# Kernel optimization log

Measured on AMD Instinct MI355X. Metric: run time of the kernel, lower is better.

Reference implementation:

```python
import jax, jax.numpy as jnp
import numpy as np

NP, NA = 200000, 100000        # paper / author node counts
EW, EC = 300000, 300000        # writes / cites edge counts
HID, H, D = 128, 4, 32         # hidden, heads, head dim
FIN_P, FIN_A, OUT = 256, 128, 16
SCALE = float(1.0 / np.sqrt(D))


def _seg_softmax(alpha, idx, n):
    # softmax over edges grouped by destination node (PyG softmax)
    m = jax.ops.segment_max(alpha, idx, num_segments=n)
    e = jnp.exp(alpha - m[idx])
    s = jax.ops.segment_sum(e, idx, num_segments=n)
    return e / (s[idx] + 1e-16)


def _edge_type(k_src, v_src, q_dst, src, dst, a_rel, m_rel, p_rel, n_dst):
    # per-relation transform at node level, then gather-attend-scatter
    kr = jnp.einsum('nhd,hde->nhe', k_src, a_rel)
    vr = jnp.einsum('nhd,hde->nhe', v_src, m_rel)
    alpha = jnp.sum(q_dst[dst] * kr[src], axis=-1) * p_rel * SCALE  # [E,H]
    alpha = _seg_softmax(alpha, dst, n_dst)
    return jax.ops.segment_sum(vr[src] * alpha[..., None], dst, num_segments=n_dst)


def setup_inputs() -> dict:
    key = jax.random.key(0)
    ks = iter(jax.random.split(key, 48))

    def nrm(shape, s=0.05):
        return jax.random.normal(next(ks), shape, jnp.float32) * s

    inp = dict(
        x_paper=nrm((NP, FIN_P), 1.0),
        x_author=nrm((NA, FIN_A), 1.0),
        writes_src=jax.random.randint(next(ks), (EW,), 0, NA, dtype=jnp.int32),
        writes_dst=jax.random.randint(next(ks), (EW,), 0, NP, dtype=jnp.int32),
        cites_src=jax.random.randint(next(ks), (EC,), 0, NP, dtype=jnp.int32),
        cites_dst=jax.random.randint(next(ks), (EC,), 0, NP, dtype=jnp.int32),
        lin_paper_w=nrm((FIN_P, HID)), lin_paper_b=jnp.zeros((HID,), jnp.float32),
        lin_author_w=nrm((FIN_A, HID)), lin_author_b=jnp.zeros((HID,), jnp.float32),
        lin_out_w=nrm((HID, OUT)), lin_out_b=jnp.zeros((OUT,), jnp.float32),
    )
    for t in ('paper', 'author'):
        for nm in ('k', 'q', 'v', 'a'):
            inp[f'{nm}_w_{t}'] = nrm((HID, HID))
            inp[f'{nm}_b_{t}'] = jnp.zeros((HID,), jnp.float32)
        inp[f'skip_{t}'] = jnp.ones((), jnp.float32)
    for e in ('writes', 'cites'):
        inp[f'a_rel_{e}'] = nrm((H, D, D), 0.18)
        inp[f'm_rel_{e}'] = nrm((H, D, D), 0.18)
        inp[f'p_rel_{e}'] = jnp.ones((H,), jnp.float32)
    return inp


def reference(x_paper, x_author, writes_src, writes_dst, cites_src, cites_dst,
              lin_paper_w, lin_paper_b, lin_author_w, lin_author_b,
              lin_out_w, lin_out_b,
              k_w_paper, k_b_paper, q_w_paper, q_b_paper, v_w_paper, v_b_paper,
              a_w_paper, a_b_paper, skip_paper,
              k_w_author, k_b_author, q_w_author, q_b_author, v_w_author, v_b_author,
              a_w_author, a_b_author, skip_author,
              a_rel_writes, m_rel_writes, p_rel_writes,
              a_rel_cites, m_rel_cites, p_rel_cites):
    # per-node-type input projection + relu
    hp = jax.nn.relu(x_paper @ lin_paper_w + lin_paper_b)
    ha = jax.nn.relu(x_author @ lin_author_w + lin_author_b)
    # HGTConv: per-node-type k/q/v, [N,H,D]
    k_p = (hp @ k_w_paper + k_b_paper).reshape(NP, H, D)
    q_p = (hp @ q_w_paper + q_b_paper).reshape(NP, H, D)
    v_p = (hp @ v_w_paper + v_b_paper).reshape(NP, H, D)
    k_a = (ha @ k_w_author + k_b_author).reshape(NA, H, D)
    v_a = (ha @ v_w_author + v_b_author).reshape(NA, H, D)
    # heterogeneous multi-relation attention, group='sum' over edge types
    out_p = _edge_type(k_a, v_a, q_p, writes_src, writes_dst,
                       a_rel_writes, m_rel_writes, p_rel_writes, NP)
    out_p = out_p + _edge_type(k_p, v_p, q_p, cites_src, cites_dst,
                               a_rel_cites, m_rel_cites, p_rel_cites, NP)
    # output projection + gated skip (paper type; only 'paper' feeds the head)
    op = jax.nn.gelu(out_p.reshape(NP, HID), approximate=False) @ a_w_paper + a_b_paper
    beta = jax.nn.sigmoid(skip_paper)
    hp = beta * op + (1.0 - beta) * hp
    return hp @ lin_out_w + lin_out_b  # [NP, OUT]
```

## Files before the change

kernel.cpp:

```cpp
#include <hip/hip_runtime.h>
#include <cstdint>

#define NP 200000
#define NA 100000
#define EW 300000
#define EC 300000
#define HID 128
#define FIN_P 256
#define FIN_A 128
#define NOUT 16
#define ATT_SCALE 0.17677669529663687f

#define NBP 1563
#define NBA 782

#define SCAN_N (2 * NP)
#define SCAN_BS 256
#define SCAN_ITEMS 4
#define SCAN_TILE 1024
#define SCAN_NB ((SCAN_N + SCAN_TILE - 1) / SCAN_TILE)

typedef short s8v __attribute__((ext_vector_type(8)));
typedef float f32x4 __attribute__((ext_vector_type(4)));
typedef unsigned short ushort_t;

__device__ __forceinline__ float gelu_f(float x) {
  return 0.5f * x * (1.0f + erff(x * 0.70710678118654752f));
}
__device__ __forceinline__ ushort_t f2bf(float f) {
  unsigned u = __float_as_uint(f);
  return (ushort_t)((u + 0x7FFFu + ((u >> 16) & 1u)) >> 16);
}
__device__ __forceinline__ unsigned pack2bf(float a, float b) {
  return (unsigned)f2bf(a) | ((unsigned)f2bf(b) << 16);
}
__device__ __forceinline__ unsigned cvtpk(float a, float b) {
  unsigned r;
  asm("v_cvt_pk_bf16_f32 %0, %1, %2" : "=v"(r) : "v"(a), "v"(b));
  return r;
}
__device__ __forceinline__ float bflo(unsigned u) { return __uint_as_float(u << 16); }
__device__ __forceinline__ float bfhi(unsigned u) { return __uint_as_float(u & 0xFFFF0000u); }

__device__ __forceinline__ void gl16(const void* g, void* l) {
  __builtin_amdgcn_global_load_lds(
      (const __attribute__((address_space(1))) void*)g,
      (__attribute__((address_space(3))) void*)l, 16, 0, 0);
}

__device__ __forceinline__ int s2row(int r) { return (r ^ (r >> 2)) & 3; }

__global__ void prep_all(
    const float* __restrict__ qw,  const float* __restrict__ qb,
    const float* __restrict__ kwp, const float* __restrict__ kbp, const float* __restrict__ arc,
    const float* __restrict__ vwp, const float* __restrict__ vbp, const float* __restrict__ mrc,
    const float* __restrict__ kwa, const float* __restrict__ kba, const float* __restrict__ arw,
    const float* __restrict__ vwa, const float* __restrict__ vba, const float* __restrict__ mrw,
    const float* __restrict__ lpw, const float* __restrict__ law,
    const float* __restrict__ aw, const float* __restrict__ ab,
    const float* __restrict__ skip, const float* __restrict__ W2, const float* __restrict__ b2,
    ushort_t* __restrict__ Wall, float* __restrict__ Ball,
    ushort_t* __restrict__ Wcatb, float* __restrict__ bo,
    int* __restrict__ cnt)
{
  const int b = blockIdx.x, tid = threadIdx.x;
  if (b == 0) {
    for (int idx = tid; idx < 16384; idx += 256) {
      int c = idx >> 7, r = idx & 127;
      Wall[idx] = f2bf(qw[r * 128 + c]);
    }
    for (int c = tid; c < 128; c += 256) Ball[c] = qb[c];
  } else if (b <= 4) {
    const float *W, *bias, *rel;
    switch (b) {
      case 1:  W = kwp; bias = kbp; rel = arc; break;
      case 2:  W = vwp; bias = vbp; rel = mrc; break;
      case 3:  W = kwa; bias = kba; rel = arw; break;
      default: W = vwa; bias = vba; rel = mrw; break;
    }
    for (int idx = tid; idx < 16384; idx += 256) {
      int c = idx >> 7, r = idx & 127, h = c >> 5, e = c & 31;
      float s = 0.f;
      #pragma unroll
      for (int d = 0; d < 32; ++d) s += W[r * 128 + h * 32 + d] * rel[h * 1024 + d * 32 + e];
      Wall[b * 16384 + idx] = f2bf(s);
    }
    for (int c = tid; c < 128; c += 256) {
      int h = c >> 5, e = c & 31;
      float s = 0.f;
      #pragma unroll
      for (int d = 0; d < 32; ++d) s += bias[h * 32 + d] * rel[h * 1024 + d * 32 + e];
      Ball[b * 128 + c] = s;
    }
  } else if (b == 5) {
    for (int idx = tid; idx < 16384; idx += 256) {
      int c = idx >> 7, r = idx & 127;
      Wall[5 * 16384 + idx] = f2bf(law[r * 128 + c]);
    }
  } else if (b == 6) {
    for (int idx = tid; idx < 32768; idx += 256) {
      int c = idx >> 8, r = idx & 255;
      Wall[6 * 16384 + idx] = f2bf(lpw[r * 128 + c]);
    }
  } else if (b == 7) {
    float beta = 1.0f / (1.0f + expf(-skip[0]));
    for (int idx = tid; idx < 4096; idx += 256) {
      int c = idx >> 8, k = idx & 255;
      float v;
      if (k < 128) {
        float s = 0.f;
        for (int j = 0; j < 128; ++j) s += aw[k * 128 + j] * W2[j * 16 + c];
        v = beta * s;
      } else {
        v = (1.0f - beta) * W2[(k - 128) * 16 + c];
      }
      Wcatb[c * 256 + k] = f2bf(v);
    }
    if (tid < 16) {
      float s = 0.f;
      for (int k = 0; k < 128; ++k) s += ab[k] * W2[k * 16 + tid];
      bo[tid] = beta * s + b2[tid];
    }
  } else {
    int chunk = SCAN_N / 8;
    int base = (b - 8) * chunk;
    for (int i = tid; i < chunk; i += 256) cnt[base + i] = 0;
  }
}

__global__ __launch_bounds__(256) void gemm_main(
    const float* __restrict__ xp, const float* __restrict__ xa,
    const ushort_t* __restrict__ Wall,
    const float* __restrict__ bp, const float* __restrict__ ba,
    const float* __restrict__ Ball,
    ushort_t* __restrict__ hpo, ushort_t* __restrict__ hao,
    ushort_t* __restrict__ qkv, ushort_t* __restrict__ kvw)
{
  __shared__ ushort_t As[16384];
  __shared__ ushort_t Bs[16384];
  const bool isP = blockIdx.x < NBP;
  const int bid = isP ? blockIdx.x : blockIdx.x - NBP;
  const float* A = isP ? xp : xa;
  const ushort_t* Wp = Wall + (isP ? 6 * 16384 : 5 * 16384);
  const float* biasp = isP ? bp : ba;
  ushort_t* Chp = isP ? hpo : hao;
  const int M = isP ? NP : NA;
  const int KT = isP ? 256 : 128;
  const int nt = KT >> 6;
  const int base_set = isP ? 0 : 3;
  const int nsets = isP ? 3 : 2;

  const int tid  = threadIdx.x;
  const int lane = tid & 63;
  const int wv   = tid >> 6;
  const int wr   = wv >> 1, wc = wv & 1;
  const int l15  = lane & 15, kgl = lane >> 4;
  const int s2l  = (l15 ^ (l15 >> 2)) & 3;
  const int row0 = bid * 128;

  const int r0 = tid >> 2, kgp = tid & 3;
  const int sk = kgp ^ s2row(r0);
  int g0 = row0 + r0;       if (g0 > M - 1) g0 = M - 1;
  int g1 = row0 + r0 + 64;  if (g1 > M - 1) g1 = M - 1;

  {
    const float* a0p = A + (size_t)g0 * KT + sk * 8;
    const float* a1p = A + (size_t)g1 * KT + sk * 8;
    const ushort_t* b0p = Wp + (size_t)r0 * KT + sk * 8;
    const ushort_t* b1p = Wp + (size_t)(r0 + 64) * KT + sk * 8;

    f32x4 acc[4][4];
    #pragma unroll
    for (int i = 0; i < 4; ++i)
      #pragma unroll
      for (int j = 0; j < 4; ++j) acc[i][j] = (f32x4){0.f, 0.f, 0.f, 0.f};

    for (int t = 0; t < nt; ++t) {
      const int kt = t * 64;
      gl16(b0p + kt,      &Bs[(size_t)tid * 8]);
      gl16(b1p + kt,      &Bs[(size_t)(tid + 256) * 8]);
      gl16(b0p + kt + 32, &Bs[(size_t)(tid + 512) * 8]);
      gl16(b1p + kt + 32, &Bs[(size_t)(tid + 768) * 8]);
      float4 fa0 = *(const float4*)(a0p + kt);
      float4 fa1 = *(const float4*)(a0p + kt + 4);
      float4 fa2 = *(const float4*)(a1p + kt);
      float4 fa3 = *(const float4*)(a1p + kt + 4);
      float4 fb0 = *(const float4*)(a0p + kt + 32);
      float4 fb1 = *(const float4*)(a0p + kt + 36);
      float4 fb2 = *(const float4*)(a1p + kt + 32);
      float4 fb3 = *(const float4*)(a1p + kt + 36);
      uint4 v;
      v.x = cvtpk(fa0.x, fa0.y); v.y = cvtpk(fa0.z, fa0.w);
      v.z = cvtpk(fa1.x, fa1.y); v.w = cvtpk(fa1.z, fa1.w);
      *(uint4*)&As[(size_t)tid * 8] = v;
      v.x = cvtpk(fa2.x, fa2.y); v.y = cvtpk(fa2.z, fa2.w);
      v.z = cvtpk(fa3.x, fa3.y); v.w = cvtpk(fa3.z, fa3.w);
      *(uint4*)&As[(size_t)(tid + 256) * 8] = v;
      v.x = cvtpk(fb0.x, fb0.y); v.y = cvtpk(fb0.z, fb0.w);
      v.z = cvtpk(fb1.x, fb1.y); v.w = cvtpk(fb1.z, fb1.w);
      *(uint4*)&As[(size_t)(tid + 512) * 8] = v;
      v.x = cvtpk(fb2.x, fb2.y); v.y = cvtpk(fb2.z, fb2.w);
      v.z = cvtpk(fb3.x, fb3.y); v.w = cvtpk(fb3.z, fb3.w);
      *(uint4*)&As[(size_t)(tid + 768) * 8] = v;
      __syncthreads();

      const s8v* As8 = (const s8v*)As;
      const s8v* Bs8 = (const s8v*)Bs;
      #pragma unroll
      for (int pg = 0; pg < 2; ++pg) {
        s8v af[4], bfv[4];
        #pragma unroll
        for (int i = 0; i < 4; ++i)
          af[i]  = As8[pg * 512 + (wr * 64 + i * 16 + l15) * 4 + (kgl ^ s2l)];
        #pragma unroll
        for (int j = 0; j < 4; ++j)
          bfv[j] = Bs8[pg * 512 + (wc * 64 + j * 16 + l15) * 4 + (kgl ^ s2l)];
        #pragma unroll
        for (int i = 0; i < 4; ++i)
          #pragma unroll
          for (int j = 0; j < 4; ++j)
            acc[i][j] = __builtin_amdgcn_mfma_f32_16x16x32_bf16(af[i], bfv[j], acc[i][j], 0, 0, 0);
      }
      __syncthreads();
    }

    float bv[4];
    #pragma unroll
    for (int j = 0; j < 4; ++j) bv[j] = biasp[wc * 64 + j * 16 + l15];
    #pragma unroll
    for (int i = 0; i < 4; ++i) {
      #pragma unroll
      for (int r = 0; r < 4; ++r) {
        int row = row0 + wr * 64 + i * 16 + kgl * 4 + r;
        if (row < M) {
          #pragma unroll
          for (int j = 0; j < 4; ++j) {
            float vv = acc[i][j][r] + bv[j];
            vv = fmaxf(vv, 0.f);
            Chp[(size_t)row * 128 + wc * 64 + j * 16 + l15] = f2bf(vv);
          }
        }
      }
    }
  }
  __syncthreads();

  {
    const ushort_t* a0h = Chp + (size_t)g0 * 128 + sk * 8;
    const ushort_t* a1h = Chp + (size_t)g1 * 128 + sk * 8;
    #pragma unroll
    for (int t = 0; t < 4; ++t) {
      gl16(a0h + t * 32, &As[((size_t)t * 512 + tid) * 8]);
      gl16(a1h + t * 32, &As[((size_t)t * 512 + tid + 256) * 8]);
    }

    for (int si = 0; si < nsets; ++si) {
      const int set = base_set + si;
      const ushort_t* W = Wall + set * 16384;
      const float* bias = Ball + set * 128;
      ushort_t* C = isP ? (qkv + (size_t)set * NP * HID)
                        : (kvw + (size_t)(set - 3) * NA * HID);
      const ushort_t* b0p = W + (size_t)r0 * 128 + sk * 8;
      const ushort_t* b1p = W + (size_t)(r0 + 64) * 128 + sk * 8;
      #pragma unroll
      for (int t = 0; t < 4; ++t) {
        gl16(b0p + t * 32, &Bs[((size_t)t * 512 + tid) * 8]);
        gl16(b1p + t * 32, &Bs[((size_t)t * 512 + tid + 256) * 8]);
      }
      __syncthreads();

      f32x4 acc[4][4];
      #pragma unroll
      for (int i = 0; i < 4; ++i)
        #pragma unroll
        for (int j = 0; j < 4; ++j) acc[i][j] = (f32x4){0.f, 0.f, 0.f, 0.f};

      const s8v* As8 = (const s8v*)As;
      const s8v* Bs8 = (const s8v*)Bs;
      #pragma unroll
      for (int t = 0; t < 4; ++t) {
        s8v af[4], bfv[4];
        #pragma unroll
        for (int i = 0; i < 4; ++i)
          af[i]  = As8[t * 512 + (wr * 64 + i * 16 + l15) * 4 + (kgl ^ s2l)];
        #pragma unroll
        for (int j = 0; j < 4; ++j)
          bfv[j] = Bs8[t * 512 + (wc * 64 + j * 16 + l15) * 4 + (kgl ^ s2l)];
        #pragma unroll
        for (int i = 0; i < 4; ++i)
          #pragma unroll
          for (int j = 0; j < 4; ++j)
            acc[i][j] = __builtin_amdgcn_mfma_f32_16x16x32_bf16(af[i], bfv[j], acc[i][j], 0, 0, 0);
      }

      float bv[4];
      #pragma unroll
      for (int j = 0; j < 4; ++j) bv[j] = bias[wc * 64 + j * 16 + l15];
      #pragma unroll
      for (int i = 0; i < 4; ++i) {
        #pragma unroll
        for (int r = 0; r < 4; ++r) {
          int row = row0 + wr * 64 + i * 16 + kgl * 4 + r;
          if (row < M) {
            #pragma unroll
            for (int j = 0; j < 4; ++j) {
              C[(size_t)row * 128 + wc * 64 + j * 16 + l15] = f2bf(acc[i][j][r] + bv[j]);
            }
          }
        }
      }
      __syncthreads();
    }
  }
}

__global__ void hist_k(const int* __restrict__ wdst, const int* __restrict__ cdst,
                       int* __restrict__ cnt)
{
  int t = blockIdx.x * blockDim.x + threadIdx.x;
  if (t < EW) atomicAdd(&cnt[wdst[t]], 1);
  if (t < EC) atomicAdd(&cnt[NP + cdst[t]], 1);
}

__global__ __launch_bounds__(SCAN_BS) void scan1(const int* __restrict__ cnt,
                                                 int* __restrict__ off,
                                                 int* __restrict__ bsum)
{
  __shared__ int sh[2][SCAN_BS];
  int tid = threadIdx.x;
  int base = blockIdx.x * SCAN_TILE + tid * SCAN_ITEMS;
  int v[SCAN_ITEMS]; int tsum = 0;
  #pragma unroll
  for (int i = 0; i < SCAN_ITEMS; ++i) {
    int idx = base + i;
    v[i] = (idx < SCAN_N) ? cnt[idx] : 0;
    tsum += v[i];
  }
  int p = 0;
  sh[0][tid] = tsum; __syncthreads();
  #pragma unroll
  for (int d = 1; d < SCAN_BS; d <<= 1) {
    int x = sh[p][tid] + ((tid >= d) ? sh[p][tid - d] : 0);
    sh[p ^ 1][tid] = x; __syncthreads(); p ^= 1;
  }
  int run = sh[p][tid] - tsum;
  #pragma unroll
  for (int i = 0; i < SCAN_ITEMS; ++i) {
    int idx = base + i;
    if (idx < SCAN_N) off[idx] = run;
    run += v[i];
  }
  if (tid == SCAN_BS - 1) bsum[blockIdx.x] = sh[p][tid];
}

__global__ __launch_bounds__(512) void scan2(int* __restrict__ bsum)
{
  __shared__ int sh[2][512];
  int tid = threadIdx.x;
  int v = (tid < SCAN_NB) ? bsum[tid] : 0;
  int p = 0;
  sh[0][tid] = v; __syncthreads();
  for (int d = 1; d < 512; d <<= 1) {
    int x = sh[p][tid] + ((tid >= d) ? sh[p][tid - d] : 0);
    sh[p ^ 1][tid] = x; __syncthreads(); p ^= 1;
  }
  if (tid < SCAN_NB) bsum[tid] = sh[p][tid] - v;
}

__global__ __launch_bounds__(SCAN_BS) void scan3(int* __restrict__ off, int* __restrict__ cur,
                                                 const int* __restrict__ bsum)
{
  int add = bsum[blockIdx.x];
  int base = blockIdx.x * SCAN_TILE + threadIdx.x;
  #pragma unroll
  for (int i = 0; i < SCAN_ITEMS; ++i) {
    int idx = base + i * SCAN_BS;
    if (idx < SCAN_N) { int t = off[idx] + add; off[idx] = t; cur[idx] = t; }
  }
  if (blockIdx.x == 0 && threadIdx.x == 0) off[SCAN_N] = EW + EC;
}

__global__ void fill_k(const int* __restrict__ wsrc, const int* __restrict__ wdst,
                       const int* __restrict__ csrc, const int* __restrict__ cdst,
                       int* __restrict__ cur, int* __restrict__ esrc)
{
  int t = blockIdx.x * blockDim.x + threadIdx.x;
  if (t < EW) { int p = atomicAdd(&cur[wdst[t]], 1); esrc[p] = wsrc[t] << 8; }
  if (t < EC) { int p = atomicAdd(&cur[NP + cdst[t]], 1); esrc[p] = csrc[t] << 8; }
}

__global__ __launch_bounds__(256) void node_attn(
    const int* __restrict__ off, const int* __restrict__ esrc,
    const ushort_t* __restrict__ q,
    const ushort_t* __restrict__ kr_w, const ushort_t* __restrict__ vr_w,
    const ushort_t* __restrict__ kr_c, const ushort_t* __restrict__ vr_c,
    const float* __restrict__ p_rel_w, const float* __restrict__ p_rel_c,
    ushort_t* __restrict__ out_p)
{
  int gid = blockIdx.x * blockDim.x + threadIdx.x;
  int node = gid >> 4;
  int l16 = gid & 15;
  int h = l16 >> 2;
  unsigned loff = (unsigned)(l16 * 16);

  int eb0 = off[node],      ee0 = off[node + 1];
  int eb1 = off[NP + node], ee1 = off[NP + node + 1];

  uint4 qv = *(const uint4*)(q + (size_t)node * HID + l16 * 8);

  int pi0 = (eb0 < ee0) ? eb0 : 0;
  int pi1 = (eb1 < ee1) ? eb1 : 0;
  unsigned pb0 = (unsigned)esrc[pi0] + loff;
  unsigned pb1 = (unsigned)esrc[pi1] + loff;
  uint4 pk[2], pv[2];
  pk[0] = *(const uint4*)((const char*)kr_w + pb0);
  pv[0] = *(const uint4*)((const char*)vr_w + pb0);
  pk[1] = *(const uint4*)((const char*)kr_c + pb1);
  pv[1] = *(const uint4*)((const char*)vr_c + pb1);

  float qf[8];
  {
    const unsigned* pq = (const unsigned*)&qv;
    #pragma unroll
    for (int w = 0; w < 4; ++w) { qf[2 * w] = bflo(pq[w]); qf[2 * w + 1] = bfhi(pq[w]); }
  }
  float prw = p_rel_w[h] * ATT_SCALE;
  float prc = p_rel_c[h] * ATT_SCALE;

  float t[8];
  #pragma unroll
  for (int i = 0; i < 8; ++i) t[i] = 0.f;

  #pragma unroll
  for (int r = 0; r < 2; ++r) {
    const char* krb = (const char*)((r == 0) ? kr_w : kr_c);
    const char* vrb = (const char*)((r == 0) ? vr_w : vr_c);
    float prr = (r == 0) ? prw : prc;
    int eb = (r == 0) ? eb0 : eb1;
    int ee = (r == 0) ? ee0 : ee1;

    float s = 0.f;
    float A[8];
    #pragma unroll
    for (int i = 0; i < 8; ++i) A[i] = 0.f;

    int e = eb;
    if (e < ee) {
      const unsigned* k8 = (const unsigned*)&pk[r];
      const unsigned* v8 = (const unsigned*)&pv[r];
      float d = 0.f;
      #pragma unroll
      for (int w = 0; w < 4; ++w) {
        d = fmaf(qf[2 * w], bflo(k8[w]), d);
        d = fmaf(qf[2 * w + 1], bfhi(k8[w]), d);
      }
      d += __shfl_xor(d, 1);
      d += __shfl_xor(d, 2);
      float p = __expf(d * prr);
      s += p;
      #pragma unroll
      for (int w = 0; w < 4; ++w) {
        A[2 * w]     = fmaf(p, bflo(v8[w]), A[2 * w]);
        A[2 * w + 1] = fmaf(p, bfhi(v8[w]), A[2 * w + 1]);
      }
      ++e;
    }
    for (; e < ee; ++e) {
      unsigned kb = (unsigned)esrc[e] + loff;
      uint4 kv = *(const uint4*)(krb + kb);
      uint4 vv = *(const uint4*)(vrb + kb);
      const unsigned* k8 = (const unsigned*)&kv;
      float d = 0.f;
      #pragma unroll
      for (int w = 0; w < 4; ++w) {
        d = fmaf(qf[2 * w], bflo(k8[w]), d);
        d = fmaf(qf[2 * w + 1], bfhi(k8[w]), d);
      }
      d += __shfl_xor(d, 1);
      d += __shfl_xor(d, 2);
      float p = __expf(d * prr);
      s += p;
      const unsigned* v8 = (const unsigned*)&vv;
      #pragma unroll
      for (int w = 0; w < 4; ++w) {
        A[2 * w]     = fmaf(p, bflo(v8[w]), A[2 * w]);
        A[2 * w + 1] = fmaf(p, bfhi(v8[w]), A[2 * w + 1]);
      }
    }
    float inv = 1.0f / (s + 1e-16f);
    #pragma unroll
    for (int i = 0; i < 8; ++i) t[i] = fmaf(A[i], inv, t[i]);
  }

  uint4 o;
  unsigned* po = (unsigned*)&o;
  #pragma unroll
  for (int w = 0; w < 4; ++w) po[w] = pack2bf(t[2 * w], t[2 * w + 1]);
  *(uint4*)(out_p + (size_t)node * HID + l16 * 8) = o;
}

__global__ __launch_bounds__(256) void epilogue_mfma(
    const ushort_t* __restrict__ out_p, const ushort_t* __restrict__ hp,
    const ushort_t* __restrict__ Wcatb, const float* __restrict__ bo,
    float* __restrict__ out)
{
  __shared__ ushort_t As[4096];
  const int tid  = threadIdx.x;
  const int lane = tid & 63;
  const int wv   = tid >> 6;
  const int l15  = lane & 15, kgl = lane >> 4;
  const int s2l  = (l15 ^ (l15 >> 2)) & 3;
  const int row0 = blockIdx.x * 128;

  const int r0 = tid >> 2, kgp = tid & 3;
  const int sk = kgp ^ s2row(r0);
  int g0 = row0 + r0;       if (g0 > NP - 1) g0 = NP - 1;
  int g1 = row0 + r0 + 64;  if (g1 > NP - 1) g1 = NP - 1;

  s8v bfr[8];
  #pragma unroll
  for (int ks = 0; ks < 8; ++ks)
    bfr[ks] = *(const s8v*)(Wcatb + (size_t)l15 * 256 + ks * 32 + kgl * 8);
  float bo_l = bo[l15];

  f32x4 acc[2];
  acc[0] = (f32x4){0.f, 0.f, 0.f, 0.f};
  acc[1] = (f32x4){0.f, 0.f, 0.f, 0.f};

  #pragma unroll
  for (int ph = 0; ph < 8; ++ph) {
    if (ph < 4) {
      const int kt = ph * 32;
      uint4 v0 = *(const uint4*)(out_p + (size_t)g0 * 128 + kt + sk * 8);
      uint4 v1 = *(const uint4*)(out_p + (size_t)g1 * 128 + kt + sk * 8);
      unsigned* p0 = (unsigned*)&v0;
      unsigned* p1 = (unsigned*)&v1;
      #pragma unroll
      for (int w = 0; w < 4; ++w) {
        p0[w] = cvtpk(gelu_f(bflo(p0[w])), gelu_f(bfhi(p0[w])));
        p1[w] = cvtpk(gelu_f(bflo(p1[w])), gelu_f(bfhi(p1[w])));
      }
      *(uint4*)&As[(size_t)tid * 8] = v0;
      *(uint4*)&As[(size_t)(tid + 256) * 8] = v1;
    } else {
      const int kt = (ph - 4) * 32;
      gl16(hp + (size_t)g0 * 128 + kt + sk * 8, &As[(size_t)tid * 8]);
      gl16(hp + (size_t)g1 * 128 + kt + sk * 8, &As[(size_t)(tid + 256) * 8]);
    }
    __syncthreads();

    const s8v* As8 = (const s8v*)As;
    s8v af0 = As8[(wv * 32 + l15) * 4 + (kgl ^ s2l)];
    s8v af1 = As8[(wv * 32 + 16 + l15) * 4 + (kgl ^ s2l)];
    acc[0] = __builtin_amdgcn_mfma_f32_16x16x32_bf16(af0, bfr[ph], acc[0], 0, 0, 0);
    acc[1] = __builtin_amdgcn_mfma_f32_16x16x32_bf16(af1, bfr[ph], acc[1], 0, 0, 0);
    __syncthreads();
  }

  #pragma unroll
  for (int i = 0; i < 2; ++i) {
    #pragma unroll
    for (int r = 0; r < 4; ++r) {
      int row = row0 + wv * 32 + i * 16 + kgl * 4 + r;
      if (row < NP) out[(size_t)row * NOUT + l15] = acc[i][r] + bo_l;
    }
  }
}

extern "C" void kernel_launch(void* const* d_in, const int* in_sizes, int n_in,
                              void* d_out, int out_size, void* d_ws, size_t ws_size,
                              hipStream_t stream)
{
  (void)in_sizes; (void)n_in; (void)out_size; (void)ws_size;
  const float* x_paper      = (const float*)d_in[0];
  const float* x_author     = (const float*)d_in[1];
  const int*   writes_src   = (const int*)d_in[2];
  const int*   writes_dst   = (const int*)d_in[3];
  const int*   cites_src    = (const int*)d_in[4];
  const int*   cites_dst    = (const int*)d_in[5];
  const float* lin_paper_w  = (const float*)d_in[6];
  const float* lin_paper_b  = (const float*)d_in[7];
  const float* lin_author_w = (const float*)d_in[8];
  const float* lin_author_b = (const float*)d_in[9];
  const float* lin_out_w    = (const float*)d_in[10];
  const float* lin_out_b    = (const float*)d_in[11];
  const float* k_w_paper    = (const float*)d_in[12];
  const float* k_b_paper    = (const float*)d_in[13];
  const float* q_w_paper    = (const float*)d_in[14];
  const float* q_b_paper    = (const float*)d_in[15];
  const float* v_w_paper    = (const float*)d_in[16];
  const float* v_b_paper    = (const float*)d_in[17];
  const float* a_w_paper    = (const float*)d_in[18];
  const float* a_b_paper    = (const float*)d_in[19];
  const float* skip_paper   = (const float*)d_in[20];
  const float* k_w_author   = (const float*)d_in[21];
  const float* k_b_author   = (const float*)d_in[22];
  const float* v_w_author   = (const float*)d_in[25];
  const float* v_b_author   = (const float*)d_in[26];
  const float* a_rel_writes = (const float*)d_in[30];
  const float* m_rel_writes = (const float*)d_in[31];
  const float* p_rel_writes = (const float*)d_in[32];
  const float* a_rel_cites  = (const float*)d_in[33];
  const float* m_rel_cites  = (const float*)d_in[34];
  const float* p_rel_cites  = (const float*)d_in[35];

  float* ws = (float*)d_ws;
  size_t off_f = 0;
  auto nxt = [&](size_t nfloats) { float* p = ws + off_f; off_f += nfloats; return p; };
  ushort_t* hp    = (ushort_t*)nxt((size_t)NP * 64);
  ushort_t* ha    = (ushort_t*)nxt((size_t)NA * 64);
  ushort_t* qkv   = (ushort_t*)nxt((size_t)3 * NP * 64);
  ushort_t* kvw   = (ushort_t*)nxt((size_t)2 * NA * 64);
  ushort_t* outp  = (ushort_t*)nxt((size_t)NP * 64);
  int*      cnt   = (int*)nxt(SCAN_N);
  int*      offs  = (int*)nxt(SCAN_N + 2);
  int*      cur   = (int*)nxt(SCAN_N);
  int*      esrc  = (int*)nxt(EW + EC);
  int*      bsum  = (int*)nxt(512);
  ushort_t* Wall  = (ushort_t*)nxt(65536);
  float*    Ball  = nxt(5 * 128);
  ushort_t* Wcatb = (ushort_t*)nxt(2048);
  float*    bo    = nxt(16);

  ushort_t* q_p  = qkv;
  ushort_t* kr_c = qkv + (size_t)NP * HID;
  ushort_t* vr_c = qkv + (size_t)2 * NP * HID;
  ushort_t* kr_w = kvw;
  ushort_t* vr_w = kvw + (size_t)NA * HID;

  prep_all<<<16, 256, 0, stream>>>(q_w_paper, q_b_paper,
                                   k_w_paper, k_b_paper, a_rel_cites,
                                   v_w_paper, v_b_paper, m_rel_cites,
                                   k_w_author, k_b_author, a_rel_writes,
                                   v_w_author, v_b_author, m_rel_writes,
                                   lin_paper_w, lin_author_w,
                                   a_w_paper, a_b_paper, skip_paper, lin_out_w, lin_out_b,
                                   Wall, Ball, Wcatb, bo, cnt);

  hist_k<<<(300000 + 255) / 256, 256, 0, stream>>>(writes_dst, cites_dst, cnt);
  scan1<<<SCAN_NB, SCAN_BS, 0, stream>>>(cnt, offs, bsum);
  scan2<<<1, 512, 0, stream>>>(bsum);
  scan3<<<SCAN_NB, SCAN_BS, 0, stream>>>(offs, cur, bsum);
  fill_k<<<(300000 + 255) / 256, 256, 0, stream>>>(writes_src, writes_dst,
                                                   cites_src, cites_dst, cur, esrc);

  gemm_main<<<NBP + NBA, 256, 0, stream>>>(x_paper, x_author, Wall,
                                           lin_paper_b, lin_author_b, Ball,
                                           hp, ha, qkv, kvw);

  node_attn<<<(NP * 16) / 256, 256, 0, stream>>>(
      offs, esrc, q_p, kr_w, vr_w, kr_c, vr_c, p_rel_writes, p_rel_cites, outp);

  epilogue_mfma<<<NBP, 256, 0, stream>>>(outp, hp, Wcatb, bo, (float*)d_out);
}
```

Measured before the change: 385.4 us.

## Halve GEMM shared-memory staging and batch attention tail edges four at a time

The second-stage GEMM now stages the hidden activations and weights in two 64-wide K phases instead of one 128-wide load. This halves the LDS footprint per block, which could allow more resident blocks, but it adds extra barriers and reloads the A tile for every weight set. The attention tail loop now gathers K/V for four edges at once with clamped indices, raising memory-level parallelism on the irregular gathers. The cost is higher register pressure and redundant loads when fewer than four edges remain.

```diff
diff --git a/kernel.cpp b/kernel.cpp
--- a/kernel.cpp
+++ b/kernel.cpp
@@ -136,8 +136,8 @@
     ushort_t* __restrict__ hpo, ushort_t* __restrict__ hao,
     ushort_t* __restrict__ qkv, ushort_t* __restrict__ kvw)
 {
-  __shared__ ushort_t As[16384];
-  __shared__ ushort_t Bs[16384];
+  __shared__ ushort_t As[8192];
+  __shared__ ushort_t Bs[8192];
   const bool isP = blockIdx.x < NBP;
   const int bid = isP ? blockIdx.x : blockIdx.x - NBP;
   const float* A = isP ? xp : xa;
@@ -248,11 +248,6 @@
   {
     const ushort_t* a0h = Chp + (size_t)g0 * 128 + sk * 8;
     const ushort_t* a1h = Chp + (size_t)g1 * 128 + sk * 8;
-    #pragma unroll
-    for (int t = 0; t < 4; ++t) {
-      gl16(a0h + t * 32, &As[((size_t)t * 512 + tid) * 8]);
-      gl16(a1h + t * 32, &As[((size_t)t * 512 + tid + 256) * 8]);
-    }
 
     for (int si = 0; si < nsets; ++si) {
       const int set = base_set + si;
@@ -262,12 +257,6 @@
                         : (kvw + (size_t)(set - 3) * NA * HID);
       const ushort_t* b0p = W + (size_t)r0 * 128 + sk * 8;
       const ushort_t* b1p = W + (size_t)(r0 + 64) * 128 + sk * 8;
-      #pragma unroll
-      for (int t = 0; t < 4; ++t) {
-        gl16(b0p + t * 32, &Bs[((size_t)t * 512 + tid) * 8]);
-        gl16(b1p + t * 32, &Bs[((size_t)t * 512 + tid + 256) * 8]);
-      }
-      __syncthreads();
 
       f32x4 acc[4][4];
       #pragma unroll
@@ -275,22 +264,37 @@
         #pragma unroll
         for (int j = 0; j < 4; ++j) acc[i][j] = (f32x4){0.f, 0.f, 0.f, 0.f};
 
-      const s8v* As8 = (const s8v*)As;
-      const s8v* Bs8 = (const s8v*)Bs;
-      #pragma unroll
-      for (int t = 0; t < 4; ++t) {
-        s8v af[4], bfv[4];
+      #pragma unroll
+      for (int ph = 0; ph < 2; ++ph) {
+        const int kt = ph * 64;
+        gl16(a0h + kt,      &As[(size_t)tid * 8]);
+        gl16(a1h + kt,      &As[(size_t)(tid + 256) * 8]);
+        gl16(a0h + kt + 32, &As[(size_t)(tid + 512) * 8]);
+        gl16(a1h + kt + 32, &As[(size_t)(tid + 768) * 8]);
+        gl16(b0p + kt,      &Bs[(size_t)tid * 8]);
+        gl16(b1p + kt,      &Bs[(size_t)(tid + 256) * 8]);
+        gl16(b0p + kt + 32, &Bs[(size_t)(tid + 512) * 8]);
+        gl16(b1p + kt + 32, &Bs[(size_t)(tid + 768) * 8]);
+        __syncthreads();
+
+        const s8v* As8 = (const s8v*)As;
+        const s8v* Bs8 = (const s8v*)Bs;
         #pragma unroll
-        for (int i = 0; i < 4; ++i)
-          af[i]  = As8[t * 512 + (wr * 64 + i * 16 + l15) * 4 + (kgl ^ s2l)];
-        #pragma unroll
-        for (int j = 0; j < 4; ++j)
-          bfv[j] = Bs8[t * 512 + (wc * 64 + j * 16 + l15) * 4 + (kgl ^ s2l)];
-        #pragma unroll
-        for (int i = 0; i < 4; ++i)
+        for (int pg = 0; pg < 2; ++pg) {
+          s8v af[4], bfv[4];
+          #pragma unroll
+          for (int i = 0; i < 4; ++i)
+            af[i]  = As8[pg * 512 + (wr * 64 + i * 16 + l15) * 4 + (kgl ^ s2l)];
           #pragma unroll
           for (int j = 0; j < 4; ++j)
-            acc[i][j] = __builtin_amdgcn_mfma_f32_16x16x32_bf16(af[i], bfv[j], acc[i][j], 0, 0, 0);
+            bfv[j] = Bs8[pg * 512 + (wc * 64 + j * 16 + l15) * 4 + (kgl ^ s2l)];
+          #pragma unroll
+          for (int i = 0; i < 4; ++i)
+            #pragma unroll
+            for (int j = 0; j < 4; ++j)
+              acc[i][j] = __builtin_amdgcn_mfma_f32_16x16x32_bf16(af[i], bfv[j], acc[i][j], 0, 0, 0);
+        }
+        __syncthreads();
       }
 
       float bv[4];
@@ -309,7 +313,6 @@
           }
         }
       }
-      __syncthreads();
     }
   }
 }
@@ -465,27 +468,50 @@
       }
       ++e;
     }
-    for (; e < ee; ++e) {
-      unsigned kb = (unsigned)esrc[e] + loff;
-      uint4 kv = *(const uint4*)(krb + kb);
-      uint4 vv = *(const uint4*)(vrb + kb);
-      const unsigned* k8 = (const unsigned*)&kv;
-      float d = 0.f;
-      #pragma unroll
-      for (int w = 0; w < 4; ++w) {
-        d = fmaf(qf[2 * w], bflo(k8[w]), d);
-        d = fmaf(qf[2 * w + 1], bfhi(k8[w]), d);
-      }
-      d += __shfl_xor(d, 1);
-      d += __shfl_xor(d, 2);
-      float p = __expf(d * prr);
-      s += p;
-      const unsigned* v8 = (const unsigned*)&vv;
-      #pragma unroll
-      for (int w = 0; w < 4; ++w) {
-        A[2 * w]     = fmaf(p, bflo(v8[w]), A[2 * w]);
-        A[2 * w + 1] = fmaf(p, bfhi(v8[w]), A[2 * w + 1]);
-      }
+    while (e < ee) {
+      int n = ee - e;
+      unsigned kb0 = (unsigned)esrc[e] + loff;
+      unsigned kb1 = (unsigned)esrc[(n > 1) ? e + 1 : e] + loff;
+      unsigned kb2 = (unsigned)esrc[(n > 2) ? e + 2 : e] + loff;
+      unsigned kb3 = (unsigned)esrc[(n > 3) ? e + 3 : e] + loff;
+      uint4 kv0 = *(const uint4*)(krb + kb0);
+      uint4 vv0 = *(const uint4*)(vrb + kb0);
+      uint4 kv1 = *(const uint4*)(krb + kb1);
+      uint4 vv1 = *(const uint4*)(vrb + kb1);
+      uint4 kv2 = *(const uint4*)(krb + kb2);
+      uint4 vv2 = *(const uint4*)(vrb + kb2);
+      uint4 kv3 = *(const uint4*)(krb + kb3);
+      uint4 vv3 = *(const uint4*)(vrb + kb3);
+      const uint4* kvs[4] = {&kv0, &kv1, &kv2, &kv3};
+      const uint4* vvs[4] = {&vv0, &vv1, &vv2, &vv3};
+      float dd[4];
+      #pragma unroll
+      for (int i = 0; i < 4; ++i) {
+        const unsigned* k8 = (const unsigned*)kvs[i];
+        float d = 0.f;
+        #pragma unroll
+        for (int w = 0; w < 4; ++w) {
+          d = fmaf(qf[2 * w], bflo(k8[w]), d);
+          d = fmaf(qf[2 * w + 1], bfhi(k8[w]), d);
+        }
+        d += __shfl_xor(d, 1);
+        d += __shfl_xor(d, 2);
+        dd[i] = d;
+      }
+      #pragma unroll
+      for (int i = 0; i < 4; ++i) {
+        if (i < n) {
+          float p = __expf(dd[i] * prr);
+          s += p;
+          const unsigned* v8 = (const unsigned*)vvs[i];
+          #pragma unroll
+          for (int w = 0; w < 4; ++w) {
+            A[2 * w]     = fmaf(p, bflo(v8[w]), A[2 * w]);
+            A[2 * w + 1] = fmaf(p, bfhi(v8[w]), A[2 * w + 1]);
+          }
+        }
+      }
+      e += 4;
     }
     float inv = 1.0f / (s + 1e-16f);
     #pragma unroll
```

Result: slower. 408.7 us (+6.0%).
